# Performance work log

Hardware: AMD Instinct MI355X
Metric: run time of the kernel (lower is better)

Reference implementation:

```python
import jax, jax.numpy as jnp
import numpy as np

B, S, D = 4, 2048, 512
H, DK, DV = 8, 64, 64


def setup_inputs() -> dict:
    key = jax.random.key(0)
    ks = jax.random.split(key, 9)
    inp = {
        "input_Q": jax.random.normal(ks[0], (B, S, D), dtype=jnp.float32),
        "input_K": jax.random.normal(ks[1], (B, S, D), dtype=jnp.float32),
        "input_V": jax.random.normal(ks[2], (B, S, D), dtype=jnp.float32),
        "attn_mask": jax.random.bernoulli(ks[3], 0.1, (B, S, S)),
        "other": jax.random.normal(ks[4], (B, S, S), dtype=jnp.float32),
        # nn.Linear weights stored [out_features, in_features]
        "W_Q": jax.random.normal(ks[5], (H * DK, D), dtype=jnp.float32) * (1.0 / np.sqrt(D)),
        "W_K": jax.random.normal(ks[6], (H * DK, D), dtype=jnp.float32) * (1.0 / np.sqrt(D)),
        "W_V": jax.random.normal(ks[7], (H * DV, D), dtype=jnp.float32) * (1.0 / np.sqrt(D)),
        "W_fc": jax.random.normal(ks[8], (D, H * DV), dtype=jnp.float32) * (1.0 / np.sqrt(H * DV)),
    }
    return inp


def reference(input_Q, input_K, input_V, attn_mask, other, W_Q, W_K, W_V, W_fc):
    b, s, _ = input_Q.shape
    # projections: y = x @ W.T, then split heads -> [B,H,S,dk]
    Q = (input_Q @ W_Q.T).reshape(b, s, H, DK).transpose(0, 2, 1, 3)
    K = (input_K @ W_K.T).reshape(b, s, H, DK).transpose(0, 2, 1, 3)
    V = (input_V @ W_V.T).reshape(b, s, H, DV).transpose(0, 2, 1, 3)
    scale = 1.0 / np.sqrt(DK).astype(np.float32)
    scores = jnp.einsum("bhqd,bhkd->bhqk", Q, K) * scale  # [B,H,S,S]
    scores = scores + other[:, None, :, :]  # additive bias broadcast over heads
    scores = jnp.where(attn_mask[:, None, :, :], jnp.float32(-1e9), scores)
    attn = jax.nn.softmax(scores, axis=-1)
    context = jnp.einsum("bhqk,bhkd->bhqd", attn, V)  # [B,H,S,DV]
    context = context.transpose(0, 2, 1, 3).reshape(b, s, H * DV)
    output = context @ W_fc.T  # dropout is identity at inference
    return (output, attn)
```

## Files before the change

### kernel.cpp

```cpp
#include <hip/hip_runtime.h>

#define BB 4
#define SS 2048
#define DDIM 512
#define HH 8
#define MTOK (BB*SS)
#define BHN (BB*HH)

typedef _Float16 f16;
typedef __attribute__((ext_vector_type(8))) _Float16 half8;
typedef __attribute__((ext_vector_type(4))) _Float16 half4;
typedef __attribute__((ext_vector_type(4))) float float4v;
typedef __attribute__((ext_vector_type(4))) int int4v;

#define SCALE_L2E 0.180336880073616f
#define L2E 1.44269504088896f
#define EBIAS 4.0f
#define MASKVAL -65504.0f

__device__ __forceinline__ float4v mfma_k32(half8 a, half8 b, float4v c) {
  return __builtin_amdgcn_mfma_f32_16x16x32_f16(a, b, c, 0, 0, 0);
}

__device__ __forceinline__ half8 cvt8(float4v a, float4v b) {
  half8 r;
  r[0] = (f16)a[0]; r[1] = (f16)a[1]; r[2] = (f16)a[2]; r[3] = (f16)a[3];
  r[4] = (f16)b[0]; r[5] = (f16)b[1]; r[6] = (f16)b[2]; r[7] = (f16)b[3];
  return r;
}

__global__ __launch_bounds__(256) void detect_mask_kernel(
    const unsigned int* __restrict__ m, unsigned int* __restrict__ flag) {
  unsigned int v = 0;
  const int base = blockIdx.x * 1024;
  for (int j = threadIdx.x; j < 1024; j += 256)
    if (m[base + j] > 1u) v = 1u;
  if (v) atomicOr(flag, 1u);
}

__global__ __launch_bounds__(256) void gemm_qkv(
    const float* __restrict__ inQ, const float* __restrict__ inK,
    const float* __restrict__ inV, const float* __restrict__ WQ,
    const float* __restrict__ WK, const float* __restrict__ WV,
    f16* __restrict__ Qp, f16* __restrict__ Kfrag, f16* __restrict__ Vfrag) {
  __shared__ f16 As[128][40];
  __shared__ f16 Bs[128][40];
  const int z = blockIdx.z;
  const float* A = (z == 0) ? inQ : (z == 1) ? inK : inV;
  const float* W = (z == 0) ? WQ : (z == 1) ? WK : WV;
  const int t = threadIdx.x;
  const int bm = blockIdx.x * 128;
  const int bn = blockIdx.y * 128;
  const int w = t >> 6, ln = t & 63;
  const int wr = w >> 1, wc = w & 1;
  const int lr = ln & 15, lg = ln >> 4;
  const int srow = t >> 1, scol = (t & 1) * 16;

  float4v acc[4][4] = {};

  for (int k0 = 0; k0 < 512; k0 += 32) {
    {
      const float* ap = A + (size_t)(bm + srow) * 512 + k0 + scol;
      float4v x0 = *(const float4v*)ap,       x1 = *(const float4v*)(ap + 4);
      float4v x2 = *(const float4v*)(ap + 8), x3 = *(const float4v*)(ap + 12);
      *(half8*)&As[srow][scol]     = cvt8(x0, x1);
      *(half8*)&As[srow][scol + 8] = cvt8(x2, x3);
    }
    {
      const float* wp = W + (size_t)(bn + srow) * 512 + k0 + scol;
      float4v x0 = *(const float4v*)wp,       x1 = *(const float4v*)(wp + 4);
      float4v x2 = *(const float4v*)(wp + 8), x3 = *(const float4v*)(wp + 12);
      *(half8*)&Bs[srow][scol]     = cvt8(x0, x1);
      *(half8*)&Bs[srow][scol + 8] = cvt8(x2, x3);
    }
    __syncthreads();
    half8 af[4], bf[4];
    #pragma unroll
    for (int m = 0; m < 4; m++) af[m] = *(const half8*)&As[wr * 64 + m * 16 + lr][lg * 8];
    #pragma unroll
    for (int n = 0; n < 4; n++) bf[n] = *(const half8*)&Bs[wc * 64 + n * 16 + lr][lg * 8];
    #pragma unroll
    for (int m = 0; m < 4; m++)
      #pragma unroll
      for (int n = 0; n < 4; n++) acc[m][n] = mfma_k32(af[m], bf[n], acc[m][n]);
    __syncthreads();
  }

  #pragma unroll
  for (int m = 0; m < 4; m++) {
    int row = bm + wr * 64 + m * 16 + lg * 4;
    #pragma unroll
    for (int n = 0; n < 4; n++) {
      int col = bn + wc * 64 + n * 16 + lr;
      int b_ = row >> 11, s_ = row & 2047, h_ = col >> 6, d_ = col & 63;
      if (z == 0) {
        #pragma unroll
        for (int r = 0; r < 4; r++)
          Qp[(size_t)(row + r) * 512 + col] = (f16)acc[m][n][r];
      } else if (z == 1) {
        #pragma unroll
        for (int r = 0; r < 4; r++) {
          int tok = s_ + r;
          Kfrag[((((size_t)(b_ * 8 + h_)) * 128 + (tok >> 4)) * 2 + (d_ >> 5)) * 512 +
                ((tok & 15) + 16 * ((d_ >> 3) & 3)) * 8 + (d_ & 7)] =
              (f16)acc[m][n][r];
        }
      } else {
        half4 ph;
        ph[0] = (f16)acc[m][n][0]; ph[1] = (f16)acc[m][n][1];
        ph[2] = (f16)acc[m][n][2]; ph[3] = (f16)acc[m][n][3];
        *(half4*)&Vfrag[((((size_t)(b_ * 8 + h_)) * 64 + (s_ >> 5)) * 4 + (d_ >> 4)) * 512 +
                        ((d_ & 15) + 16 * ((s_ >> 2) & 3)) * 8 + ((s_ >> 2) & 4)] = ph;
      }
    }
  }
}

__global__ __launch_bounds__(256) void gemm_out(const f16* __restrict__ ctx,
                                                const float* __restrict__ W,
                                                float* __restrict__ Out) {
  __shared__ f16 As[128][40];
  __shared__ f16 Bs[128][40];
  const int t = threadIdx.x;
  const int bm = blockIdx.x * 128;
  const int bn = blockIdx.y * 128;
  const int w = t >> 6, ln = t & 63;
  const int wr = w >> 1, wc = w & 1;
  const int lr = ln & 15, lg = ln >> 4;
  const int srow = t >> 1, scol = (t & 1) * 16;

  float4v acc[4][4] = {};

  for (int k0 = 0; k0 < 512; k0 += 32) {
    {
      const f16* ap = ctx + (size_t)(bm + srow) * 512 + k0 + scol;
      *(half8*)&As[srow][scol]     = *(const half8*)(ap);
      *(half8*)&As[srow][scol + 8] = *(const half8*)(ap + 8);
    }
    {
      const float* wp = W + (size_t)(bn + srow) * 512 + k0 + scol;
      float4v x0 = *(const float4v*)wp,       x1 = *(const float4v*)(wp + 4);
      float4v x2 = *(const float4v*)(wp + 8), x3 = *(const float4v*)(wp + 12);
      *(half8*)&Bs[srow][scol]     = cvt8(x0, x1);
      *(half8*)&Bs[srow][scol + 8] = cvt8(x2, x3);
    }
    __syncthreads();
    half8 af[4], bf[4];
    #pragma unroll
    for (int m = 0; m < 4; m++) af[m] = *(const half8*)&As[wr * 64 + m * 16 + lr][lg * 8];
    #pragma unroll
    for (int n = 0; n < 4; n++) bf[n] = *(const half8*)&Bs[wc * 64 + n * 16 + lr][lg * 8];
    #pragma unroll
    for (int m = 0; m < 4; m++)
      #pragma unroll
      for (int n = 0; n < 4; n++) acc[m][n] = mfma_k32(af[m], bf[n], acc[m][n]);
    __syncthreads();
  }

  #pragma unroll
  for (int m = 0; m < 4; m++) {
    int row = bm + wr * 64 + m * 16 + lg * 4;
    #pragma unroll
    for (int n = 0; n < 4; n++) {
      int col = bn + wc * 64 + n * 16 + lr;
      #pragma unroll
      for (int r = 0; r < 4; r++)
        Out[(size_t)(row + r) * 512 + col] = acc[m][n][r];
    }
  }
}

#define LOADT(dst, base, st) {                                  \
    const f16* p_ = (base) + (size_t)(st) * 2048;               \
    dst##0 = *(const half8*)(p_);                               \
    dst##1 = *(const half8*)(p_ + 512);                         \
    dst##2 = *(const half8*)(p_ + 1024);                        \
    dst##3 = *(const half8*)(p_ + 1536); }

__global__ __launch_bounds__(1024) void attn_fused(
    const f16* __restrict__ Qp, const f16* __restrict__ Kfrag,
    const f16* __restrict__ Vfrag, const float* __restrict__ other,
    const unsigned char* __restrict__ mask8, const int* __restrict__ mask32,
    const unsigned int* __restrict__ flag, float* __restrict__ attn_out,
    f16* __restrict__ ctx) {
  __shared__ float red[16][16];
  __shared__ float red2[16][16][66];

  const int t = threadIdx.x;
  const int bid = blockIdx.x;
  const int b = bid & 3;
  const int qblk = (bid >> 2) * 16;
  const int w = t >> 6, ln = t & 63;
  const int lr = ln & 15, lg = ln >> 4;
  const bool use8 = (*flag) != 0;

  const int q_g = qblk + lr;
  const f16* kfb = Kfrag + (size_t)(b * 8) * 131072 + ln * 8;
  const f16* vfb = Vfrag + (size_t)(b * 8) * 131072 + ln * 8;
  const f16* qpp = Qp + ((size_t)b * SS + q_g) * 512 + lg * 8;

  half8 o0, o1, o2, o3;
  #define OLOAD(dst, g) {                                                 \
    const size_t ob_ = ((size_t)b * SS + q_g) * SS + w * 128 + (g) * 32 + lg * 4; \
    float4v x0 = *(const float4v*)&other[ob_];                            \
    float4v x1 = *(const float4v*)&other[ob_ + 16];                       \
    float4v r0, r1;                                                       \
    if (use8) {                                                           \
      unsigned int m0 = *(const unsigned int*)&mask8[ob_];                \
      unsigned int m1 = *(const unsigned int*)&mask8[ob_ + 16];           \
      _Pragma("unroll")                                                   \
      for (int r = 0; r < 4; r++) {                                       \
        r0[r] = ((m0 >> (8 * r)) & 0xffu) ? MASKVAL : fmaf(x0[r], L2E, -EBIAS); \
        r1[r] = ((m1 >> (8 * r)) & 0xffu) ? MASKVAL : fmaf(x1[r], L2E, -EBIAS); \
      }                                                                   \
    } else {                                                              \
      int4v m0 = *(const int4v*)&mask32[ob_];                             \
      int4v m1 = *(const int4v*)&mask32[ob_ + 16];                        \
      _Pragma("unroll")                                                   \
      for (int r = 0; r < 4; r++) {                                       \
        r0[r] = m0[r] ? MASKVAL : fmaf(x0[r], L2E, -EBIAS);               \
        r1[r] = m1[r] ? MASKVAL : fmaf(x1[r], L2E, -EBIAS);               \
      }                                                                   \
    }                                                                     \
    dst = cvt8(r0, r1);                                                   \
  }
  OLOAD(o0, 0);
  OLOAD(o1, 1);
  OLOAD(o2, 2);
  OLOAD(o3, 3);
  #undef OLOAD

  half8 kA0, kA1, kA2, kA3, kB0, kB1, kB2, kB3;
  half8 vf0, vf1, vf2, vf3;

  LOADT(kA, kfb, w * 4 + 0);

  #define BODY(kf, oreg, edst) {                                          \
    float4v s0 = {}, s1 = {};                                             \
    s0 = mfma_k32(kf##0, qf0, s0);                                        \
    s0 = mfma_k32(kf##1, qf1, s0);                                        \
    s1 = mfma_k32(kf##2, qf0, s1);                                        \
    s1 = mfma_k32(kf##3, qf1, s1);                                        \
    float4v ev0, ev1;                                                     \
    _Pragma("unroll")                                                     \
    for (int r = 0; r < 4; r++) {                                         \
      ev0[r] = exp2f(fmaf(s0[r], SCALE_L2E, (float)oreg[r]));             \
      ev1[r] = exp2f(fmaf(s1[r], SCALE_L2E, (float)oreg[4 + r]));         \
    }                                                                     \
    rs += (ev0[0] + ev0[1]) + (ev0[2] + ev0[3]) +                         \
          (ev1[0] + ev1[1]) + (ev1[2] + ev1[3]);                          \
    edst = cvt8(ev0, ev1);                                                \
    cacc0 = mfma_k32(edst, vf0, cacc0);                                   \
    cacc1 = mfma_k32(edst, vf1, cacc1);                                   \
    cacc2 = mfma_k32(edst, vf2, cacc2);                                   \
    cacc3 = mfma_k32(edst, vf3, cacc3);                                   \
  }

  #define ASTORE(e, g) {                                                  \
    float4v av0, av1;                                                     \
    av0[0] = (float)e[0] * invl; av0[1] = (float)e[1] * invl;             \
    av0[2] = (float)e[2] * invl; av0[3] = (float)e[3] * invl;             \
    av1[0] = (float)e[4] * invl; av1[1] = (float)e[5] * invl;             \
    av1[2] = (float)e[6] * invl; av1[3] = (float)e[7] * invl;             \
    *(float4v*)(abase + (g) * 32 + lg * 4) = av0;                         \
    *(float4v*)(abase + (g) * 32 + 16 + lg * 4) = av1;                    \
  }

  for (int h = 0; h < 8; ++h) {
    const int bh = b * 8 + h;
    const f16* kfb_nx = (h < 7) ? kfb + 131072 : kfb;

    half8 qf0 = *(const half8*)(qpp + h * 64);
    half8 qf1 = *(const half8*)(qpp + h * 64 + 32);

    float rs = 0.f;
    float4v cacc0 = {}, cacc1 = {}, cacc2 = {}, cacc3 = {};
    half8 e0, e1, e2, e3;

    LOADT(vf, vfb, w * 4 + 0);
    LOADT(kB, kfb, w * 4 + 1);
    BODY(kA, o0, e0);

    LOADT(vf, vfb, w * 4 + 1);
    LOADT(kA, kfb, w * 4 + 2);
    BODY(kB, o1, e1);

    LOADT(vf, vfb, w * 4 + 2);
    LOADT(kB, kfb, w * 4 + 3);
    BODY(kA, o2, e2);

    LOADT(vf, vfb, w * 4 + 3);
    LOADT(kA, kfb_nx, w * 4 + 0);
    BODY(kB, o3, e3);

    rs += __shfl_xor(rs, 16);
    rs += __shfl_xor(rs, 32);
    if (ln < 16) red[w][lr] = rs;
    #pragma unroll
    for (int r = 0; r < 4; r++) {
      red2[w][lg * 4 + r][0 * 16 + lr] = cacc0[r];
      red2[w][lg * 4 + r][1 * 16 + lr] = cacc1[r];
      red2[w][lg * 4 + r][2 * 16 + lr] = cacc2[r];
      red2[w][lg * 4 + r][3 * 16 + lr] = cacc3[r];
    }
    __syncthreads();

    float lsum = 0.f;
    #pragma unroll
    for (int ww = 0; ww < 16; ww++) lsum += red[ww][lr];
    const float invl = 1.0f / lsum;

    float* abase = attn_out + ((size_t)bh * SS + q_g) * SS + w * 128;
    ASTORE(e0, 0);
    ASTORE(e1, 1);
    ASTORE(e2, 2);
    ASTORE(e3, 3);

    {
      float s16 = 0.f, l2 = 0.f;
      #pragma unroll
      for (int ww = 0; ww < 16; ww++) {
        s16 += red2[ww][w][ln];
        l2 += red[ww][w];
      }
      ctx[((size_t)b * SS + qblk + w) * 512 + h * 64 + ln] = (f16)(s16 / l2);
    }
    __syncthreads();

    kfb = kfb_nx;
    vfb = (h < 7) ? vfb + 131072 : vfb;
  }
  #undef BODY
  #undef ASTORE
}

extern "C" void kernel_launch(void* const* d_in, const int* in_sizes, int n_in,
                              void* d_out, int out_size, void* d_ws, size_t ws_size,
                              hipStream_t stream) {
  const float* inQ   = (const float*)d_in[0];
  const float* inK   = (const float*)d_in[1];
  const float* inV   = (const float*)d_in[2];
  const void*  mask  = d_in[3];
  const float* other = (const float*)d_in[4];
  const float* WQ    = (const float*)d_in[5];
  const float* WK    = (const float*)d_in[6];
  const float* WV    = (const float*)d_in[7];
  const float* WF    = (const float*)d_in[8];

  char* ws = (char*)d_ws;
  size_t off = 0;
  unsigned int* flag = (unsigned int*)(ws + off); off += 256;
  f16* Qp    = (f16*)(ws + off); off += (size_t)MTOK * 512 * 2;
  f16* Kfrag = (f16*)(ws + off); off += (size_t)MTOK * 512 * 2;
  f16* Vfrag = (f16*)(ws + off); off += (size_t)MTOK * 512 * 2;
  f16* ctx   = (f16*)(ws + off); off += (size_t)MTOK * 512 * 2;
  if (ws_size < off) return;

  float* outp  = (float*)d_out;
  float* attnp = outp + (size_t)MTOK * DDIM;

  hipMemsetAsync(flag, 0, 256, stream);
  detect_mask_kernel<<<64, 256, 0, stream>>>((const unsigned int*)mask, flag);

  gemm_qkv<<<dim3(64, 4, 3), 256, 0, stream>>>(inQ, inK, inV, WQ, WK, WV,
                                               Qp, Kfrag, Vfrag);

  attn_fused<<<512, 1024, 0, stream>>>(
      Qp, Kfrag, Vfrag, other, (const unsigned char*)mask, (const int*)mask,
      flag, attnp, ctx);

  gemm_out<<<dim3(64, 4), 256, 0, stream>>>(ctx, WF, outp);
}
```

Baseline: 399.1 us.

## Split attention blocks per head instead of looping heads inside each block

Each block now handles a single (batch, head, 16-query) tile with 8 waves covering 256 keys each, instead of one 16-wave block iterating over all 8 heads. This removes the per-head loop and its two block-wide barriers and raises the block count for better occupancy and latency hiding. In exchange, the bias and mask tile is reloaded once per head rather than reused across heads, which adds global read traffic. Launch bounds change to 512 threads with a minimum of 4 blocks.

```diff
diff --git a/kernel.cpp b/kernel.cpp
--- a/kernel.cpp
+++ b/kernel.cpp
@@ -177,31 +177,35 @@
     dst##2 = *(const half8*)(p_ + 1024);                        \
     dst##3 = *(const half8*)(p_ + 1536); }
 
-__global__ __launch_bounds__(1024) void attn_fused(
+__global__ __launch_bounds__(512, 4) void attn_fused(
     const f16* __restrict__ Qp, const f16* __restrict__ Kfrag,
     const f16* __restrict__ Vfrag, const float* __restrict__ other,
     const unsigned char* __restrict__ mask8, const int* __restrict__ mask32,
     const unsigned int* __restrict__ flag, float* __restrict__ attn_out,
     f16* __restrict__ ctx) {
-  __shared__ float red[16][16];
-  __shared__ float red2[16][16][66];
+  __shared__ float red[8][16];
+  __shared__ float red2[8][16][66];
 
   const int t = threadIdx.x;
   const int bid = blockIdx.x;
-  const int b = bid & 3;
-  const int qblk = (bid >> 2) * 16;
+  const int bh = bid & 31;
+  const int qblk = (bid >> 5) * 16;
+  const int b = bh >> 3, h = bh & 7;
   const int w = t >> 6, ln = t & 63;
   const int lr = ln & 15, lg = ln >> 4;
   const bool use8 = (*flag) != 0;
 
   const int q_g = qblk + lr;
-  const f16* kfb = Kfrag + (size_t)(b * 8) * 131072 + ln * 8;
-  const f16* vfb = Vfrag + (size_t)(b * 8) * 131072 + ln * 8;
-  const f16* qpp = Qp + ((size_t)b * SS + q_g) * 512 + lg * 8;
-
-  half8 o0, o1, o2, o3;
+  const f16* kfb = Kfrag + (size_t)bh * 131072 + ln * 8;
+  const f16* vfb = Vfrag + (size_t)bh * 131072 + ln * 8;
+
+  const f16* qpp = Qp + ((size_t)b * SS + q_g) * 512 + h * 64 + lg * 8;
+  const half8 qf0 = *(const half8*)(qpp);
+  const half8 qf1 = *(const half8*)(qpp + 32);
+
+  half8 o0, o1, o2, o3, o4, o5, o6, o7;
   #define OLOAD(dst, g) {                                                 \
-    const size_t ob_ = ((size_t)b * SS + q_g) * SS + w * 128 + (g) * 32 + lg * 4; \
+    const size_t ob_ = ((size_t)b * SS + q_g) * SS + w * 256 + (g) * 32 + lg * 4; \
     float4v x0 = *(const float4v*)&other[ob_];                            \
     float4v x1 = *(const float4v*)&other[ob_ + 16];                       \
     float4v r0, r1;                                                       \
@@ -224,16 +228,15 @@
     }                                                                     \
     dst = cvt8(r0, r1);                                                   \
   }
-  OLOAD(o0, 0);
-  OLOAD(o1, 1);
-  OLOAD(o2, 2);
-  OLOAD(o3, 3);
+  OLOAD(o0, 0); OLOAD(o1, 1); OLOAD(o2, 2); OLOAD(o3, 3);
+  OLOAD(o4, 4); OLOAD(o5, 5); OLOAD(o6, 6); OLOAD(o7, 7);
   #undef OLOAD
 
   half8 kA0, kA1, kA2, kA3, kB0, kB1, kB2, kB3;
   half8 vf0, vf1, vf2, vf3;
-
-  LOADT(kA, kfb, w * 4 + 0);
+  half8 e0, e1, e2, e3, e4, e5, e6, e7;
+  float rs = 0.f;
+  float4v cacc0 = {}, cacc1 = {}, cacc2 = {}, cacc3 = {};
 
   #define BODY(kf, oreg, edst) {                                          \
     float4v s0 = {}, s1 = {};                                             \
@@ -256,6 +259,55 @@
     cacc3 = mfma_k32(edst, vf3, cacc3);                                   \
   }
 
+  const int s0i = w * 8;
+  LOADT(kA, kfb, s0i + 0);
+  LOADT(vf, vfb, s0i + 0);
+
+  LOADT(kB, kfb, s0i + 1);
+  BODY(kA, o0, e0);
+  LOADT(vf, vfb, s0i + 1);
+  LOADT(kA, kfb, s0i + 2);
+  BODY(kB, o1, e1);
+  LOADT(vf, vfb, s0i + 2);
+  LOADT(kB, kfb, s0i + 3);
+  BODY(kA, o2, e2);
+  LOADT(vf, vfb, s0i + 3);
+  LOADT(kA, kfb, s0i + 4);
+  BODY(kB, o3, e3);
+  LOADT(vf, vfb, s0i + 4);
+  LOADT(kB, kfb, s0i + 5);
+  BODY(kA, o4, e4);
+  LOADT(vf, vfb, s0i + 5);
+  LOADT(kA, kfb, s0i + 6);
+  BODY(kB, o5, e5);
+  LOADT(vf, vfb, s0i + 6);
+  LOADT(kB, kfb, s0i + 7);
+  BODY(kA, o6, e6);
+  LOADT(vf, vfb, s0i + 7);
+  BODY(kB, o7, e7);
+  #undef BODY
+
+  {
+    float v = rs;
+    v += __shfl_xor(v, 16);
+    v += __shfl_xor(v, 32);
+    if (ln < 16) red[w][lr] = v;
+  }
+  #pragma unroll
+  for (int r = 0; r < 4; r++) {
+    red2[w][lg * 4 + r][0 * 16 + lr] = cacc0[r];
+    red2[w][lg * 4 + r][1 * 16 + lr] = cacc1[r];
+    red2[w][lg * 4 + r][2 * 16 + lr] = cacc2[r];
+    red2[w][lg * 4 + r][3 * 16 + lr] = cacc3[r];
+  }
+  __syncthreads();
+
+  float lsum = 0.f;
+  #pragma unroll
+  for (int ww = 0; ww < 8; ww++) lsum += red[ww][lr];
+  const float invl = 1.0f / lsum;
+
+  float* abase = attn_out + ((size_t)bh * SS + q_g) * SS + w * 256;
   #define ASTORE(e, g) {                                                  \
     float4v av0, av1;                                                     \
     av0[0] = (float)e[0] * invl; av0[1] = (float)e[1] * invl;             \
@@ -265,73 +317,25 @@
     *(float4v*)(abase + (g) * 32 + lg * 4) = av0;                         \
     *(float4v*)(abase + (g) * 32 + 16 + lg * 4) = av1;                    \
   }
-
-  for (int h = 0; h < 8; ++h) {
-    const int bh = b * 8 + h;
-    const f16* kfb_nx = (h < 7) ? kfb + 131072 : kfb;
-
-    half8 qf0 = *(const half8*)(qpp + h * 64);
-    half8 qf1 = *(const half8*)(qpp + h * 64 + 32);
-
-    float rs = 0.f;
-    float4v cacc0 = {}, cacc1 = {}, cacc2 = {}, cacc3 = {};
-    half8 e0, e1, e2, e3;
-
-    LOADT(vf, vfb, w * 4 + 0);
-    LOADT(kB, kfb, w * 4 + 1);
-    BODY(kA, o0, e0);
-
-    LOADT(vf, vfb, w * 4 + 1);
-    LOADT(kA, kfb, w * 4 + 2);
-    BODY(kB, o1, e1);
-
-    LOADT(vf, vfb, w * 4 + 2);
-    LOADT(kB, kfb, w * 4 + 3);
-    BODY(kA, o2, e2);
-
-    LOADT(vf, vfb, w * 4 + 3);
-    LOADT(kA, kfb_nx, w * 4 + 0);
-    BODY(kB, o3, e3);
-
-    rs += __shfl_xor(rs, 16);
-    rs += __shfl_xor(rs, 32);
-    if (ln < 16) red[w][lr] = rs;
-    #pragma unroll
-    for (int r = 0; r < 4; r++) {
-      red2[w][lg * 4 + r][0 * 16 + lr] = cacc0[r];
-      red2[w][lg * 4 + r][1 * 16 + lr] = cacc1[r];
-      red2[w][lg * 4 + r][2 * 16 + lr] = cacc2[r];
-      red2[w][lg * 4 + r][3 * 16 + lr] = cacc3[r];
-    }
-    __syncthreads();
-
-    float lsum = 0.f;
-    #pragma unroll
-    for (int ww = 0; ww < 16; ww++) lsum += red[ww][lr];
-    const float invl = 1.0f / lsum;
-
-    float* abase = attn_out + ((size_t)bh * SS + q_g) * SS + w * 128;
-    ASTORE(e0, 0);
-    ASTORE(e1, 1);
-    ASTORE(e2, 2);
-    ASTORE(e3, 3);
-
-    {
-      float s16 = 0.f, l2 = 0.f;
-      #pragma unroll
-      for (int ww = 0; ww < 16; ww++) {
-        s16 += red2[ww][w][ln];
-        l2 += red[ww][w];
-      }
-      ctx[((size_t)b * SS + qblk + w) * 512 + h * 64 + ln] = (f16)(s16 / l2);
-    }
-    __syncthreads();
-
-    kfb = kfb_nx;
-    vfb = (h < 7) ? vfb + 131072 : vfb;
-  }
-  #undef BODY
+  ASTORE(e0, 0); ASTORE(e1, 1); ASTORE(e2, 2); ASTORE(e3, 3);
+  ASTORE(e4, 4); ASTORE(e5, 5); ASTORE(e6, 6); ASTORE(e7, 7);
   #undef ASTORE
+
+  {
+    const int q = t >> 5;
+    const int dv0 = (t & 31) * 2;
+    float l_c = 0.f, c0 = 0.f, c1 = 0.f;
+    #pragma unroll
+    for (int ww = 0; ww < 8; ww++) {
+      l_c += red[ww][q];
+      c0 += red2[ww][q][dv0];
+      c1 += red2[ww][q][dv0 + 1];
+    }
+    const float invc = 1.0f / l_c;
+    f16* cp = ctx + ((size_t)b * SS + qblk + q) * 512 + h * 64 + dv0;
+    cp[0] = (f16)(c0 * invc);
+    cp[1] = (f16)(c1 * invc);
+  }
 }
 
 extern "C" void kernel_launch(void* const* d_in, const int* in_sizes, int n_in,
@@ -365,7 +369,7 @@
   gemm_qkv<<<dim3(64, 4, 3), 256, 0, stream>>>(inQ, inK, inV, WQ, WK, WV,
                                                Qp, Kfrag, Vfrag);
 
-  attn_fused<<<512, 1024, 0, stream>>>(
+  attn_fused<<<4096, 512, 0, stream>>>(
       Qp, Kfrag, Vfrag, other, (const unsigned char*)mask, (const int*)mask,
       flag, attnp, ctx);
 
```

Result: slower. 493.0 us (+23.5%).
